# Kernel tuning notes

Measured on AMD Instinct MI355X. Metric: run time of the kernel, lower is better.

The kernel has to match this reference:

```python
import jax, jax.numpy as jnp
import numpy as np

N_NODES = 50000
N_EDGES = 800000
D = 128            # in_channels == hidden_channels
N_LAYERS = 3
OUT = 16
N_GRAPHS = 128


def setup_inputs() -> dict:
    key = jax.random.key(0)
    ks = jax.random.split(key, 12)
    x = jax.random.normal(ks[0], (N_NODES, D), dtype=jnp.float32)
    edge_index = jax.random.randint(ks[1], (2, N_EDGES), 0, N_NODES, dtype=jnp.int64)
    batch_ids = jnp.sort(jax.random.randint(ks[2], (N_NODES,), 0, N_GRAPHS, dtype=jnp.int64))
    s = 1.0 / np.sqrt(D)
    # Stacked per-layer GraphConv weights (all layers are D->D here).
    Wrel = jax.random.uniform(ks[3], (N_LAYERS, D, D), jnp.float32, -s, s)
    brel = jax.random.uniform(ks[4], (N_LAYERS, D), jnp.float32, -s, s)
    Wroot = jax.random.uniform(ks[5], (N_LAYERS, D, D), jnp.float32, -s, s)
    # post_mp MLP head
    W1 = jax.random.uniform(ks[6], (D, D), jnp.float32, -s, s)
    b1 = jax.random.uniform(ks[7], (D,), jnp.float32, -s, s)
    W2 = jax.random.uniform(ks[8], (D, OUT), jnp.float32, -s, s)
    b2 = jax.random.uniform(ks[9], (OUT,), jnp.float32, -s, s)
    return {"x": x, "edge_index": edge_index, "batch_ids": batch_ids,
            "Wrel": Wrel, "brel": brel, "Wroot": Wroot,
            "W1": W1, "b1": b1, "W2": W2, "b2": b2}


def reference(x, edge_index, batch_ids, Wrel, brel, Wroot, W1, b1, W2, b2):
    src, dst = edge_index[0], edge_index[1]
    h = x
    for l in range(N_LAYERS):
        # GraphConv: lin_rel(sum_{j->i} h_j) + lin_root(h_i)
        agg = jax.ops.segment_sum(h[src], dst, num_segments=N_NODES)  # [N, D]
        h = agg @ Wrel[l] + brel[l] + h @ Wroot[l]
        h = jax.nn.relu(h)
        # dropout p=0.0 / eval mode -> identity
    # global mean pool over graphs
    sums = jax.ops.segment_sum(h, batch_ids, num_segments=N_GRAPHS)          # [G, D]
    counts = jax.ops.segment_sum(jnp.ones((N_NODES,), h.dtype), batch_ids,
                                 num_segments=N_GRAPHS)                       # [G]
    pooled = sums / jnp.maximum(counts, 1.0)[:, None]
    # post_mp MLP (dropout identity in eval)
    out = (pooled @ W1 + b1) @ W2 + b2                                        # [G, OUT]
    return out
```

## Files before the change

### kernel.cpp

```cpp
#include <hip/hip_runtime.h>

#define N_NODES 50000
#define N_EDGES 800000
#define D 128
#define N_LAYERS 3
#define OUT_F 16
#define N_GRAPHS 128
#define NBUCK 391
#define EPB 4096
#define NB3 ((N_EDGES + EPB - 1) / EPB)
#define CAP 4096
#define NT32 ((N_NODES + 31) / 32)
#define PITCH 132
#define NCAST 6250
#define NPREPW 96

typedef __attribute__((ext_vector_type(8))) short short8;
typedef __attribute__((ext_vector_type(16))) float floatx16;

__device__ __forceinline__ unsigned short f2bf(float f) {
  unsigned int u = __float_as_uint(f);
  u += 0x7fff + ((u >> 16) & 1);
  return (unsigned short)(u >> 16);
}
__device__ __forceinline__ float bf2f(unsigned short b) {
  return __uint_as_float(((unsigned int)b) << 16);
}
__device__ __forceinline__ float blo(unsigned v) { return __uint_as_float(v << 16); }
__device__ __forceinline__ float bhi(unsigned v) { return __uint_as_float(v & 0xffff0000u); }

__global__ __launch_bounds__(256) void partition_kernel(
    const int* __restrict__ src, const int* __restrict__ dst,
    int* __restrict__ cursor, unsigned* __restrict__ pairs) {
  __shared__ unsigned pk[EPB];
  __shared__ int hist[NBUCK];
  __shared__ int wcur[NBUCK];
  const int e0 = blockIdx.x * EPB;
  const int n = min(EPB, N_EDGES - e0);
  const int t = threadIdx.x;
  for (int i = t; i < NBUCK; i += 256) hist[i] = 0;
  __syncthreads();
  for (int i = t; i < n; i += 256) {
    int d = dst[e0 + i], s = src[e0 + i];
    pk[i] = ((unsigned)d << 16) | (unsigned)s;
    atomicAdd(&hist[d >> 7], 1);
  }
  __syncthreads();
  for (int i = t; i < NBUCK; i += 256)
    wcur[i] = i * CAP + (hist[i] ? atomicAdd(&cursor[i], hist[i]) : 0);
  __syncthreads();
  for (int i = t; i < n; i += 256) {
    unsigned p = pk[i];
    int pos = atomicAdd(&wcur[p >> 23], 1);
    pairs[pos] = p;
  }
}

__global__ __launch_bounds__(256) void bucket_sort_kernel(
    const unsigned* __restrict__ pairs, const int* __restrict__ cursor,
    int* __restrict__ rowbeg, int* __restrict__ rowend, int* __restrict__ esrc) {
  __shared__ unsigned pk[CAP];
  __shared__ int sorted[CAP];
  __shared__ int hist[128], off[128], cur[128];
  const int bkt = blockIdx.x;
  const int t = threadIdx.x;
  const int beg = bkt * CAP;
  const int cnt = cursor[bkt];
  if (t < 128) hist[t] = 0;
  __syncthreads();
  for (int i = t; i < cnt; i += 256) {
    unsigned p = pairs[beg + i];
    pk[i] = p;
    atomicAdd(&hist[(p >> 16) & 127], 1);
  }
  __syncthreads();
  if (t < 128) off[t] = hist[t];
  __syncthreads();
  for (int o = 1; o < 128; o <<= 1) {
    int x = (t < 128 && t >= o) ? off[t - o] : 0;
    __syncthreads();
    if (t < 128) off[t] += x;
    __syncthreads();
  }
  if (t < 128) {
    int node = bkt * 128 + t;
    if (node < N_NODES) {
      rowbeg[node] = beg + off[t] - hist[t];
      rowend[node] = beg + off[t];
    }
    cur[t] = off[t] - hist[t];
  }
  __syncthreads();
  for (int i = t; i < cnt; i += 256) {
    unsigned p = pk[i];
    int pos = atomicAdd(&cur[(p >> 16) & 127], 1);
    sorted[pos] = (int)(p & 0xFFFFu);
  }
  __syncthreads();
  for (int i = t; i < cnt; i += 256) esrc[beg + i] = sorted[i];
}

__global__ __launch_bounds__(256) void prep_all_kernel(
    const float* __restrict__ x, unsigned short* __restrict__ x16,
    const float* __restrict__ Wrel, const float* __restrict__ Wroot,
    unsigned short* __restrict__ wt, int* __restrict__ cursor) {
  const int bid = blockIdx.x;
  const int t = threadIdx.x;
  if (bid < NCAST) {
    const int i = bid * 256 + t;
    const float4 v = *(const float4*)&x[(size_t)i * 4];
    uint2 o;
    o.x = f2bf(v.x) | ((unsigned)f2bf(v.y) << 16);
    o.y = f2bf(v.z) | ((unsigned)f2bf(v.w) << 16);
    *(uint2*)&x16[(size_t)i * 4] = o;
  } else if (bid < NCAST + NPREPW) {
    const int idx = (bid - NCAST) * 256 + t;
    const int lane = idx & 63;
    const int kst = (idx >> 6) & 31;
    const int nt = (idx >> 11) & 1;
    const int half = (idx >> 12) & 1;
    const int l = idx >> 13;
    const int n = half * 64 + nt * 32 + (lane & 31);
    const int kx0 = kst * 16 + (lane >> 5) * 8;
    const int seg = kx0 >> 7;
    const int k0 = kx0 & 127;
    const int mat = seg >> 1, lo = seg & 1;
    const float* W = (mat ? Wroot : Wrel) + (size_t)l * D * D;
    unsigned short v[8];
#pragma unroll
    for (int j = 0; j < 8; ++j) {
      float w = W[(size_t)(k0 + j) * D + n];
      unsigned short hi = f2bf(w);
      v[j] = lo ? f2bf(w - bf2f(hi)) : hi;
    }
    unsigned short* dstp =
        wt + ((size_t)l * 128 + (half * 2 + nt) * 32 + kst) * 512 + lane * 8;
    *(uint4*)dstp = *(const uint4*)v;
  } else {
    const int i = (bid - NCAST - NPREPW) * 256 + t;
    if (i < NBUCK) cursor[i] = 0;
  }
}

__global__ __launch_bounds__(256) void agg_kernel(
    const unsigned short* __restrict__ h,
    const int* __restrict__ rowbeg, const int* __restrict__ rowend,
    const int* __restrict__ esrc, unsigned short* __restrict__ agg) {
  const int idx = blockIdx.x * 256 + threadIdx.x;
  const int n = idx >> 4;
  const int lane = idx & 15;
  if (n >= N_NODES) return;
  const int beg = rowbeg[n], end = rowend[n];
  float a0 = 0, a1 = 0, a2 = 0, a3 = 0, a4 = 0, a5 = 0, a6 = 0, a7 = 0;
  int e = beg;
  for (; e + 4 <= end; e += 4) {
    const int s0 = esrc[e],     s1 = esrc[e + 1];
    const int s2 = esrc[e + 2], s3 = esrc[e + 3];
    const uint4 v0 = *(const uint4*)&h[(size_t)s0 * D + lane * 8];
    const uint4 v1 = *(const uint4*)&h[(size_t)s1 * D + lane * 8];
    const uint4 v2 = *(const uint4*)&h[(size_t)s2 * D + lane * 8];
    const uint4 v3 = *(const uint4*)&h[(size_t)s3 * D + lane * 8];
    a0 += blo(v0.x) + blo(v1.x) + blo(v2.x) + blo(v3.x);
    a1 += bhi(v0.x) + bhi(v1.x) + bhi(v2.x) + bhi(v3.x);
    a2 += blo(v0.y) + blo(v1.y) + blo(v2.y) + blo(v3.y);
    a3 += bhi(v0.y) + bhi(v1.y) + bhi(v2.y) + bhi(v3.y);
    a4 += blo(v0.z) + blo(v1.z) + blo(v2.z) + blo(v3.z);
    a5 += bhi(v0.z) + bhi(v1.z) + bhi(v2.z) + bhi(v3.z);
    a6 += blo(v0.w) + blo(v1.w) + blo(v2.w) + blo(v3.w);
    a7 += bhi(v0.w) + bhi(v1.w) + bhi(v2.w) + bhi(v3.w);
  }
  for (; e < end; ++e) {
    const int s0 = esrc[e];
    const uint4 v0 = *(const uint4*)&h[(size_t)s0 * D + lane * 8];
    a0 += blo(v0.x); a1 += bhi(v0.x);
    a2 += blo(v0.y); a3 += bhi(v0.y);
    a4 += blo(v0.z); a5 += bhi(v0.z);
    a6 += blo(v0.w); a7 += bhi(v0.w);
  }
  uint4 o;
  o.x = f2bf(a0) | ((unsigned)f2bf(a1) << 16);
  o.y = f2bf(a2) | ((unsigned)f2bf(a3) << 16);
  o.z = f2bf(a4) | ((unsigned)f2bf(a5) << 16);
  o.w = f2bf(a6) | ((unsigned)f2bf(a7) << 16);
  *(uint4*)&agg[(size_t)n * D + lane * 8] = o;
}

__global__ __launch_bounds__(512, 8) void gemm_kernel(
    const unsigned short* __restrict__ agg, const unsigned short* __restrict__ hv,
    const unsigned short* __restrict__ wt,
    const float* __restrict__ brel,
    unsigned short* __restrict__ outp) {
  __shared__ unsigned short atile[32 * PITCH];
  __shared__ unsigned short htile[32 * PITCH];
  __shared__ float redB[4][16][64];
  const int t = threadIdx.x;
  const int r0 = blockIdx.x * 32;
  const int g = t >> 4, li = t & 15;
  const int row = r0 + g;
  if (row < N_NODES) {
    *(uint4*)&htile[g * PITCH + li * 8] =
        *(const uint4*)&hv[(size_t)row * D + li * 8];
    *(uint4*)&atile[g * PITCH + li * 8] =
        *(const uint4*)&agg[(size_t)row * D + li * 8];
  } else {
    const uint4 z = {0, 0, 0, 0};
    *(uint4*)&htile[g * PITCH + li * 8] = z;
    *(uint4*)&atile[g * PITCH + li * 8] = z;
  }
  __syncthreads();

  const int wave = t >> 6, lane = t & 63;
  const int p = wave & 3, chain = wave >> 2;
  const int r2 = lane & 31, hseg = lane >> 5;
  const unsigned short* tile = chain ? htile : atile;
  short8 fr[8];
#pragma unroll
  for (int i = 0; i < 8; ++i)
    fr[i] = *(const short8*)&tile[r2 * PITCH + i * 16 + hseg * 8];
  const unsigned short* ws = wt + (size_t)(p * 32 + chain * 16) * 512;
  floatx16 acc = {0.f};
#pragma unroll
  for (int k = 0; k < 16; ++k) {
    const short8 b = *(const short8*)&ws[(size_t)k * 512 + lane * 8];
    acc = __builtin_amdgcn_mfma_f32_32x32x16_bf16(fr[k & 7], b, acc, 0, 0, 0);
  }
  if (chain) {
#pragma unroll
    for (int reg = 0; reg < 16; ++reg) redB[p][reg][lane] = acc[reg];
  }
  __syncthreads();
  if (!chain) {
    const int cb = p * 32 + r2;
    const float bias = brel[cb];
#pragma unroll
    for (int reg = 0; reg < 16; ++reg) {
      const int orow = r0 + (reg & 3) + 8 * (reg >> 2) + 4 * hseg;
      if (orow < N_NODES)
        outp[(size_t)orow * D + cb] =
            f2bf(fmaxf(acc[reg] + redB[p][reg][lane] + bias, 0.f));
    }
  }
}

__device__ __forceinline__ int lb_search(const int* __restrict__ a, int n, int key) {
  int lo = 0, hi = n;
  while (lo < hi) {
    int m = (lo + hi) >> 1;
    if (a[m] < key) lo = m + 1; else hi = m;
  }
  return lo;
}

__global__ __launch_bounds__(256) void pool_head_kernel(
    const unsigned short* __restrict__ h, const int* __restrict__ batch,
    const float* __restrict__ W1, const float* __restrict__ b1,
    const float* __restrict__ W2, const float* __restrict__ b2,
    float* __restrict__ out) {
  __shared__ float sums_lds[16][128];
  __shared__ float pooled[128];
  __shared__ float hidden[128];
  __shared__ int range[2];
  const int g = blockIdx.x;
  const int t = threadIdx.x;
  if (t < 2) range[t] = lb_search(batch, N_NODES, g + t);
  __syncthreads();
  const int lo = range[0], hi = range[1];
  const int rg = t >> 4, cg = t & 15;
  float a0 = 0, a1 = 0, a2 = 0, a3 = 0, a4 = 0, a5 = 0, a6 = 0, a7 = 0;
  for (int n = lo + rg; n < hi; n += 16) {
    const uint4 v = *(const uint4*)&h[(size_t)n * D + cg * 8];
    a0 += blo(v.x); a1 += bhi(v.x);
    a2 += blo(v.y); a3 += bhi(v.y);
    a4 += blo(v.z); a5 += bhi(v.z);
    a6 += blo(v.w); a7 += bhi(v.w);
  }
  sums_lds[rg][cg * 8 + 0] = a0; sums_lds[rg][cg * 8 + 1] = a1;
  sums_lds[rg][cg * 8 + 2] = a2; sums_lds[rg][cg * 8 + 3] = a3;
  sums_lds[rg][cg * 8 + 4] = a4; sums_lds[rg][cg * 8 + 5] = a5;
  sums_lds[rg][cg * 8 + 6] = a6; sums_lds[rg][cg * 8 + 7] = a7;
  __syncthreads();
  if (t < 128) {
    float s = 0.f;
#pragma unroll
    for (int r = 0; r < 16; ++r) s += sums_lds[r][t];
    pooled[t] = s / fmaxf((float)(hi - lo), 1.f);
  }
  __syncthreads();
  if (t < 128) {
    float a = b1[t];
    for (int k = 0; k < D; ++k) a += pooled[k] * W1[k * D + t];
    hidden[t] = a;
  }
  __syncthreads();
  if (t < OUT_F) {
    float o = b2[t];
    for (int k = 0; k < D; ++k) o += hidden[k] * W2[k * OUT_F + t];
    out[(size_t)g * OUT_F + t] = o;
  }
}

extern "C" void kernel_launch(void* const* d_in, const int* in_sizes, int n_in,
                              void* d_out, int out_size, void* d_ws, size_t ws_size,
                              hipStream_t stream) {
  const float* x     = (const float*)d_in[0];
  const int*   ei    = (const int*)d_in[1];
  const int*   batch = (const int*)d_in[2];
  const float* Wrel  = (const float*)d_in[3];
  const float* brel  = (const float*)d_in[4];
  const float* Wroot = (const float*)d_in[5];
  const float* W1    = (const float*)d_in[6];
  const float* b1    = (const float*)d_in[7];
  const float* W2    = (const float*)d_in[8];
  const float* b2    = (const float*)d_in[9];
  float* out = (float*)d_out;

  const size_t ND = (size_t)N_NODES * D;
  unsigned short* bufA = (unsigned short*)d_ws;
  unsigned short* bufB = bufA + ND;
  unsigned short* bufC = bufB + ND;
  unsigned short* wt   = bufC + ND;
  int* rowbeg = (int*)(wt + (size_t)N_LAYERS * 128 * 512);
  int* rowend = rowbeg + N_NODES;
  int* esrc   = rowend + N_NODES;
  unsigned* pairs = (unsigned*)(esrc + (size_t)NBUCK * CAP);
  int* cursor = (int*)(pairs + (size_t)NBUCK * CAP);

  const int* esrc_in = ei;
  const int* edst_in = ei + N_EDGES;

  prep_all_kernel<<<NCAST + NPREPW + 2, 256, 0, stream>>>(
      x, bufC, Wrel, Wroot, wt, cursor);
  partition_kernel<<<NB3, 256, 0, stream>>>(esrc_in, edst_in, cursor, pairs);
  bucket_sort_kernel<<<NBUCK, 256, 0, stream>>>(pairs, cursor, rowbeg, rowend, esrc);

  const size_t WL = (size_t)128 * 512;
  const int agg_blocks = (N_NODES * 16 + 255) / 256;
  agg_kernel<<<agg_blocks, 256, 0, stream>>>(bufC, rowbeg, rowend, esrc, bufB);
  gemm_kernel<<<NT32, 512, 0, stream>>>(bufB, bufC, wt, brel, bufA);
  agg_kernel<<<agg_blocks, 256, 0, stream>>>(bufA, rowbeg, rowend, esrc, bufB);
  gemm_kernel<<<NT32, 512, 0, stream>>>(bufB, bufA, wt + WL, brel + D, bufC);
  agg_kernel<<<agg_blocks, 256, 0, stream>>>(bufC, rowbeg, rowend, esrc, bufB);
  gemm_kernel<<<NT32, 512, 0, stream>>>(bufB, bufC, wt + 2 * WL, brel + 2 * D, bufA);

  pool_head_kernel<<<N_GRAPHS, 256, 0, stream>>>(bufA, batch, W1, b1, W2, b2, out);
}
```

Before: 283.3 us.

## Restructure GEMM so each wave owns a 32-row tile with LDS-staged weights

The GEMM kernel changes from one 32-row tile per block, where 8 waves split output columns and the two input chains and then reduce through LDS, to 8 row tiles per block. Each wave keeps both the agg and h fragments for its own tile in registers and runs the full K=256 chain itself, which removes the cross-wave reduction. The weights are staged into 64KB of LDS in two halves and shared by all 8 waves, replacing per-wave global weight loads. The cost is a large LDS footprint, lower occupancy (launch bounds drop from 8 to 2), many block-wide barriers, and serialized staging loops.

```diff
diff --git a/kernel.cpp b/kernel.cpp
--- a/kernel.cpp
+++ b/kernel.cpp
@@ -11,6 +11,7 @@
 #define NB3 ((N_EDGES + EPB - 1) / EPB)
 #define CAP 4096
 #define NT32 ((N_NODES + 31) / 32)
+#define NGB ((NT32 + 7) / 8)
 #define PITCH 132
 #define NCAST 6250
 #define NPREPW 96
@@ -185,60 +186,72 @@
   *(uint4*)&agg[(size_t)n * D + lane * 8] = o;
 }
 
-__global__ __launch_bounds__(512, 8) void gemm_kernel(
+__global__ __launch_bounds__(512, 2) void gemm_kernel(
     const unsigned short* __restrict__ agg, const unsigned short* __restrict__ hv,
     const unsigned short* __restrict__ wt,
     const float* __restrict__ brel,
     unsigned short* __restrict__ outp) {
-  __shared__ unsigned short atile[32 * PITCH];
-  __shared__ unsigned short htile[32 * PITCH];
-  __shared__ float redB[4][16][64];
-  const int t = threadIdx.x;
-  const int r0 = blockIdx.x * 32;
+  __shared__ unsigned short lds[32768];
+  const int t = threadIdx.x;
+  const int wave = t >> 6, lane = t & 63;
   const int g = t >> 4, li = t & 15;
-  const int row = r0 + g;
-  if (row < N_NODES) {
-    *(uint4*)&htile[g * PITCH + li * 8] =
-        *(const uint4*)&hv[(size_t)row * D + li * 8];
-    *(uint4*)&atile[g * PITCH + li * 8] =
-        *(const uint4*)&agg[(size_t)row * D + li * 8];
-  } else {
-    const uint4 z = {0, 0, 0, 0};
-    *(uint4*)&htile[g * PITCH + li * 8] = z;
-    *(uint4*)&atile[g * PITCH + li * 8] = z;
-  }
-  __syncthreads();
-
-  const int wave = t >> 6, lane = t & 63;
-  const int p = wave & 3, chain = wave >> 2;
   const int r2 = lane & 31, hseg = lane >> 5;
-  const unsigned short* tile = chain ? htile : atile;
-  short8 fr[8];
-#pragma unroll
-  for (int i = 0; i < 8; ++i)
-    fr[i] = *(const short8*)&tile[r2 * PITCH + i * 16 + hseg * 8];
-  const unsigned short* ws = wt + (size_t)(p * 32 + chain * 16) * 512;
-  floatx16 acc = {0.f};
-#pragma unroll
-  for (int k = 0; k < 16; ++k) {
-    const short8 b = *(const short8*)&ws[(size_t)k * 512 + lane * 8];
-    acc = __builtin_amdgcn_mfma_f32_32x32x16_bf16(fr[k & 7], b, acc, 0, 0, 0);
-  }
-  if (chain) {
-#pragma unroll
-    for (int reg = 0; reg < 16; ++reg) redB[p][reg][lane] = acc[reg];
-  }
-  __syncthreads();
-  if (!chain) {
-    const int cb = p * 32 + r2;
-    const float bias = brel[cb];
-#pragma unroll
-    for (int reg = 0; reg < 16; ++reg) {
-      const int orow = r0 + (reg & 3) + 8 * (reg >> 2) + 4 * hseg;
-      if (orow < N_NODES)
-        outp[(size_t)orow * D + cb] =
-            f2bf(fmaxf(acc[reg] + redB[p][reg][lane] + bias, 0.f));
-    }
+  const int tile = blockIdx.x * 8 + wave;
+
+  short8 ag[8], hh[8];
+#pragma unroll
+  for (int r = 0; r < 4; ++r) {
+#pragma unroll
+    for (int j = 0; j < 4; ++j) {
+      int srow = (blockIdx.x * 8 + 2 * r + (j >> 1)) * 32 + g;
+      if (srow >= N_NODES) srow = N_NODES - 1;
+      const unsigned short* sp = (j & 1) ? hv : agg;
+      *(uint4*)&lds[(j * 32 + g) * PITCH + li * 8] =
+          *(const uint4*)&sp[(size_t)srow * D + li * 8];
+    }
+    __syncthreads();
+    if ((wave >> 1) == r) {
+      const int slot = wave & 1;
+#pragma unroll
+      for (int i = 0; i < 8; ++i) {
+        ag[i] = *(const short8*)&lds[(slot * 2 + 0) * 32 * PITCH +
+                                     r2 * PITCH + i * 16 + hseg * 8];
+        hh[i] = *(const short8*)&lds[(slot * 2 + 1) * 32 * PITCH +
+                                     r2 * PITCH + i * 16 + hseg * 8];
+      }
+    }
+    __syncthreads();
+  }
+
+  const int r0 = tile * 32;
+#pragma unroll
+  for (int pp = 0; pp < 2; ++pp) {
+    const unsigned short* ws = wt + (size_t)pp * 32768;
+#pragma unroll
+    for (int j = 0; j < 8; ++j) {
+      const int idx = t + j * 512;
+      *(uint4*)&lds[idx * 8] = *(const uint4*)&ws[idx * 8];
+    }
+    __syncthreads();
+#pragma unroll
+    for (int p2 = 0; p2 < 2; ++p2) {
+      floatx16 acc = {0.f};
+#pragma unroll
+      for (int kst = 0; kst < 32; ++kst) {
+        const short8 af = (kst < 16) ? ag[kst & 7] : hh[kst & 7];
+        const short8 b = *(const short8*)&lds[(p2 * 32 + kst) * 512 + lane * 8];
+        acc = __builtin_amdgcn_mfma_f32_32x32x16_bf16(af, b, acc, 0, 0, 0);
+      }
+      const int cb = (pp * 2 + p2) * 32 + r2;
+      const float bias = brel[cb];
+#pragma unroll
+      for (int reg = 0; reg < 16; ++reg) {
+        const int orow = r0 + (reg & 3) + 8 * (reg >> 2) + 4 * hseg;
+        if (orow < N_NODES)
+          outp[(size_t)orow * D + cb] = f2bf(fmaxf(acc[reg] + bias, 0.f));
+      }
+    }
+    __syncthreads();
   }
 }
 
@@ -336,11 +349,11 @@
   const size_t WL = (size_t)128 * 512;
   const int agg_blocks = (N_NODES * 16 + 255) / 256;
   agg_kernel<<<agg_blocks, 256, 0, stream>>>(bufC, rowbeg, rowend, esrc, bufB);
-  gemm_kernel<<<NT32, 512, 0, stream>>>(bufB, bufC, wt, brel, bufA);
+  gemm_kernel<<<NGB, 512, 0, stream>>>(bufB, bufC, wt, brel, bufA);
   agg_kernel<<<agg_blocks, 256, 0, stream>>>(bufA, rowbeg, rowend, esrc, bufB);
-  gemm_kernel<<<NT32, 512, 0, stream>>>(bufB, bufA, wt + WL, brel + D, bufC);
+  gemm_kernel<<<NGB, 512, 0, stream>>>(bufB, bufA, wt + WL, brel + D, bufC);
   agg_kernel<<<agg_blocks, 256, 0, stream>>>(bufC, rowbeg, rowend, esrc, bufB);
-  gemm_kernel<<<NT32, 512, 0, stream>>>(bufB, bufC, wt + 2 * WL, brel + 2 * D, bufA);
+  gemm_kernel<<<NGB, 512, 0, stream>>>(bufB, bufC, wt + 2 * WL, brel + 2 * D, bufA);
 
   pool_head_kernel<<<N_GRAPHS, 256, 0, stream>>>(bufA, batch, W1, b1, W2, b2, out);
 }
```

New measurement: 277.3 us. 1.02x faster.
